# Kernel optimization log

Hardware: AMD Instinct MI355X
Metric: run time of the kernel (lower is better)

## Reference

```python
import jax, jax.numpy as jnp
import numpy as np

N, E, D, ED, H, OUT = 50000, 800000, 128, 32, 16, 128
BN_EPS = 1e-5


def setup_inputs() -> dict:
    key = jax.random.key(0)
    ks = jax.random.split(key, 12)
    s = lambda fan_in: 1.0 / np.sqrt(fan_in)

    x = jax.random.normal(ks[0], (N, D), dtype=jnp.float32)
    edge_idx = jax.random.randint(ks[1], (2, E), 0, N, dtype=jnp.int64)
    edge_feat = jax.random.normal(ks[2], (E, ED), dtype=jnp.float32)

    # edge_mlp: Linear(ED,16) -> GELU -> Linear(16,16); weights stored [in,out]
    eW1 = jax.random.uniform(ks[3], (ED, H), minval=-s(ED), maxval=s(ED), dtype=jnp.float32)
    eb1 = jnp.zeros((H,), jnp.float32)
    eW2 = jax.random.uniform(ks[4], (H, H), minval=-s(H), maxval=s(H), dtype=jnp.float32)
    eb2 = jnp.zeros((H,), jnp.float32)

    # ego_proj: Linear(D, D+16, bias=False)
    ego_W = jax.random.uniform(ks[5], (D, D + H), minval=-s(D), maxval=s(D), dtype=jnp.float32)
    eps = jnp.zeros((1,), jnp.float32)

    # node mlp: Linear(D+16, OUT) -> BN(OUT) -> GELU -> Linear(OUT, OUT)
    W1 = jax.random.uniform(ks[6], (D + H, OUT), minval=-s(D + H), maxval=s(D + H), dtype=jnp.float32)
    b1 = jnp.zeros((OUT,), jnp.float32)
    gamma = jnp.ones((OUT,), jnp.float32)
    beta = jnp.zeros((OUT,), jnp.float32)
    W2 = jax.random.uniform(ks[7], (OUT, OUT), minval=-s(OUT), maxval=s(OUT), dtype=jnp.float32)
    b2 = jnp.zeros((OUT,), jnp.float32)

    return dict(x=x, edge_idx=edge_idx, edge_feat=edge_feat,
                eW1=eW1, eb1=eb1, eW2=eW2, eb2=eb2,
                ego_W=ego_W, eps=eps,
                W1=W1, b1=b1, gamma=gamma, beta=beta, W2=W2, b2=b2)


def reference(x, edge_idx, edge_feat, eW1, eb1, eW2, eb2, ego_W, eps,
              W1, b1, gamma, beta, W2, b2):
    src, dst = edge_idx[0], edge_idx[1]
    # edge MLP (exact GELU, matching torch default)
    e_emb = jax.nn.gelu(edge_feat @ eW1 + eb1, approximate=False) @ eW2 + eb2  # [E,16]
    msg = jnp.concatenate([x[src], e_emb], axis=-1)                            # [E, D+16]
    agg = jax.ops.segment_sum(msg, dst, num_segments=x.shape[0])               # [N, D+16]
    out = (1.0 + eps) * (x @ ego_W) + agg
    # node MLP with BatchNorm1d in training mode (batch stats, biased var)
    h = out @ W1 + b1
    mu = jnp.mean(h, axis=0)
    var = jnp.mean((h - mu) ** 2, axis=0)
    h = (h - mu) * jax.lax.rsqrt(var + BN_EPS) * gamma + beta
    h = jax.nn.gelu(h, approximate=False)
    return h @ W2 + b2
```

## Files before the change

kernel.cpp:

```cpp
#include <hip/hip_runtime.h>
#include <hip/hip_bf16.h>

#define N_NODES 50000
#define E_EDGES 800000
#define D_IN    128
#define ED_IN   32
#define H_HID   16
#define D_CAT   144
#define AGG_LD  144
#define BCAP    48
#define BM      64
#define EDGE_BLKS (E_EDGES / 256)

typedef __attribute__((ext_vector_type(8))) short bf16x8;
typedef __attribute__((ext_vector_type(4))) float f32x4;

__device__ __forceinline__ float gelu_exact(float v) {
    return 0.5f * v * (1.0f + erff(v * 0.70710678118654752f));
}
__device__ __forceinline__ float4 ld4(const float* p) { return *reinterpret_cast<const float4*>(p); }
__device__ __forceinline__ unsigned short f2bf(float f) {
    unsigned u = __float_as_uint(f);
    return (unsigned short)((u + 0x7FFFu + ((u >> 16) & 1u)) >> 16);
}
__device__ __forceinline__ float bflo(unsigned u) { return __uint_as_float(u << 16); }
__device__ __forceinline__ float bfhi(unsigned u) { return __uint_as_float(u & 0xffff0000u); }
__device__ __forceinline__ unsigned packbf2(float lo, float hi) {
    __hip_bfloat162 h = __float22bfloat162_rn(make_float2(lo, hi));
    return *reinterpret_cast<unsigned*>(&h);
}

__global__ __launch_bounds__(256) void k_zero(int* __restrict__ cnt, float* __restrict__ stats) {
    int i = blockIdx.x * 256 + threadIdx.x;
    if (i < 12500) *reinterpret_cast<int4*>(cnt + i * 4) = make_int4(0, 0, 0, 0);
    if (blockIdx.x == 49 && threadIdx.x < 64)
        *reinterpret_cast<float4*>(stats + threadIdx.x * 4) = make_float4(0.f, 0.f, 0.f, 0.f);
}

__global__ __launch_bounds__(256) void k_edge(const float* __restrict__ x,
        uint4* __restrict__ xb, const int* __restrict__ eidx,
        const float* __restrict__ ef, const float* __restrict__ eW1,
        const float* __restrict__ eb1,
        const float* __restrict__ egoW, const float* __restrict__ W1,
        const float* __restrict__ eps, const float* __restrict__ eW2,
        const float* __restrict__ eb2, const float* __restrict__ W2,
        int* __restrict__ cnt, int* __restrict__ bucket,
        unsigned short* __restrict__ gbuf, unsigned short* __restrict__ BT,
        unsigned short* __restrict__ W2T, float* __restrict__ ve) {
    const int b = blockIdx.x, t = threadIdx.x;
    if (b >= EDGE_BLKS) {
        if (t >= 128) return;
        const int c = t;
        const int d = b - EDGE_BLKS;
        if (d < 128) {
            float acc = 0.f;
            for (int j = 0; j < D_CAT; ++j)
                acc = fmaf(egoW[d * D_CAT + j], W1[j * 128 + c], acc);
            BT[c * 288 + d] = f2bf((1.0f + eps[0]) * acc);
        } else if (d == 128) {
            for (int j = 0; j < 128; ++j)
                BT[c * 288 + 128 + j] = f2bf(W1[j * 128 + c]);
            #pragma unroll
            for (int j = 0; j < H_HID; ++j) {
                float s = 0.f;
                #pragma unroll
                for (int k = 0; k < H_HID; ++k)
                    s = fmaf(eW2[j * H_HID + k], W1[(D_IN + k) * 128 + c], s);
                BT[c * 288 + 256 + j] = f2bf(s);
            }
            #pragma unroll
            for (int j = 272; j < 288; ++j) BT[c * 288 + j] = 0;
            float s = 0.f;
            #pragma unroll
            for (int k = 0; k < H_HID; ++k)
                s = fmaf(eb2[k], W1[(D_IN + k) * 128 + c], s);
            ve[c] = s;
        } else {
            for (int k = 0; k < 128; ++k)
                W2T[c * 128 + k] = f2bf(W2[k * 128 + c]);
        }
        return;
    }
    const int e0 = b * 256;
    const int i = e0 + t;
    const int w = t >> 6, l = t & 63, q = l >> 4, c = l & 15;
    const int eb = e0 + w * 64;

    float4 cx0 = ld4(x + (size_t)i * 8);
    float4 cx1 = ld4(x + (size_t)i * 8 + 4);
    int dst = eidx[E_EDGES + i];
    float4 ef0[4], ef1[4];
    #pragma unroll
    for (int m = 0; m < 4; ++m) {
        const float* ep = ef + (size_t)(eb + m * 16 + c) * ED_IN + q * 8;
        ef0[m] = ld4(ep);
        ef1[m] = ld4(ep + 4);
    }
    float wv[8];
    #pragma unroll
    for (int j = 0; j < 8; ++j) wv[j] = eW1[(q * 8 + j) * 16 + c];
    union { uint4 u; bf16x8 v; } afc;
    afc.u.x = packbf2(wv[0], wv[1]); afc.u.y = packbf2(wv[2], wv[3]);
    afc.u.z = packbf2(wv[4], wv[5]); afc.u.w = packbf2(wv[6], wv[7]);
    const bf16x8 af = afc.v;
    float bias[4];
    #pragma unroll
    for (int j = 0; j < 4; ++j) bias[j] = eb1[q * 4 + j];

    {
        uint4 o;
        o.x = packbf2(cx0.x, cx0.y); o.y = packbf2(cx0.z, cx0.w);
        o.z = packbf2(cx1.x, cx1.y); o.w = packbf2(cx1.z, cx1.w);
        xb[i] = o;
    }
    {
        int pos = atomicAdd(&cnt[dst], 1);
        if (pos < BCAP) bucket[dst * BCAP + pos] = i;
    }
    #pragma unroll
    for (int m = 0; m < 4; ++m) {
        const int em = eb + m * 16 + c;
        union { uint4 u; bf16x8 v; } bc;
        bc.u.x = packbf2(ef0[m].x, ef0[m].y); bc.u.y = packbf2(ef0[m].z, ef0[m].w);
        bc.u.z = packbf2(ef1[m].x, ef1[m].y); bc.u.w = packbf2(ef1[m].z, ef1[m].w);
        f32x4 acc = (f32x4){0.f, 0.f, 0.f, 0.f};
        acc = __builtin_amdgcn_mfma_f32_16x16x32_bf16(af, bc.v, acc, 0, 0, 0);
        uint2 o;
        o.x = packbf2(gelu_exact(acc[0] + bias[0]), gelu_exact(acc[1] + bias[1]));
        o.y = packbf2(gelu_exact(acc[2] + bias[2]), gelu_exact(acc[3] + bias[3]));
        *reinterpret_cast<uint2*>(gbuf + (size_t)em * 16 + q * 4) = o;
    }
}

__global__ __launch_bounds__(256) void k_agg(const unsigned short* __restrict__ xb,
        const int* __restrict__ eidx, const int* __restrict__ cnt,
        const int* __restrict__ bucket, const unsigned short* __restrict__ gbuf,
        unsigned short* __restrict__ aggb) {
    const int wave = threadIdx.x >> 6, lane = threadIdx.x & 63;
    const int q = lane >> 4, ql = lane & 15;
    const int n = blockIdx.x * 4 + wave;
    const int m = min(cnt[n], BCAP);
    int ev = (lane < BCAP) ? bucket[n * BCAP + lane] : 0;
    int sv = (lane < m) ? eidx[ev] : 0;
    float a[8], ae[8];
    #pragma unroll
    for (int i = 0; i < 8; ++i) { a[i] = 0.f; ae[i] = 0.f; }
    const int ng = (m + 3) >> 2;
    #pragma unroll 4
    for (int j = 0; j < ng; ++j) {
        const int eo = 4 * j + q;
        const int s  = __shfl(sv, eo);
        const int ge = __shfl(ev, eo);
        if (eo < m) {
            uint4 v = *reinterpret_cast<const uint4*>(xb + (size_t)s * D_IN + ql * 8);
            a[0] += bflo(v.x); a[1] += bfhi(v.x);
            a[2] += bflo(v.y); a[3] += bfhi(v.y);
            a[4] += bflo(v.z); a[5] += bfhi(v.z);
            a[6] += bflo(v.w); a[7] += bfhi(v.w);
            if (ql < 2) {
                uint4 e = *reinterpret_cast<const uint4*>(gbuf + (size_t)ge * 16 + ql * 8);
                ae[0] += bflo(e.x); ae[1] += bfhi(e.x);
                ae[2] += bflo(e.y); ae[3] += bfhi(e.y);
                ae[4] += bflo(e.z); ae[5] += bfhi(e.z);
                ae[6] += bflo(e.w); ae[7] += bfhi(e.w);
            }
        }
    }
    #pragma unroll
    for (int i = 0; i < 8; ++i) {
        a[i]  += __shfl_xor(a[i], 16);  a[i]  += __shfl_xor(a[i], 32);
        ae[i] += __shfl_xor(ae[i], 16); ae[i] += __shfl_xor(ae[i], 32);
    }
    if (q == 0) {
        unsigned short* ar = aggb + (size_t)n * AGG_LD;
        uint4 o;
        o.x = packbf2(a[0], a[1]); o.y = packbf2(a[2], a[3]);
        o.z = packbf2(a[4], a[5]); o.w = packbf2(a[6], a[7]);
        *reinterpret_cast<uint4*>(ar + ql * 8) = o;
        if (ql < 2) {
            uint4 oe;
            oe.x = packbf2(ae[0], ae[1]); oe.y = packbf2(ae[2], ae[3]);
            oe.z = packbf2(ae[4], ae[5]); oe.w = packbf2(ae[6], ae[7]);
            *reinterpret_cast<uint4*>(ar + D_IN + ql * 8) = oe;
        }
    }
}

__global__ __launch_bounds__(256) void k_gemm1(const unsigned short* __restrict__ xb,
        const unsigned short* __restrict__ aggb, const unsigned short* __restrict__ BT,
        const float* __restrict__ ve, const int* __restrict__ cnt,
        float* __restrict__ h, float* __restrict__ stats) {
    __shared__ short As[64][40];
    __shared__ short Bs[128][40];
    __shared__ float red0[128], red1[128];
    __shared__ float ve_s[128];
    __shared__ int   deg_s[64];
    const int t = threadIdx.x;
    const int row0 = blockIdx.x * BM;
    if (t < 128) { ve_s[t] = ve[t]; red0[t] = 0.f; red1[t] = 0.f; }
    if (t < 64) deg_s[t] = cnt[min(row0 + t, N_NODES - 1)];
    const int w = t >> 6, l = t & 63;
    const int arow = w * 16 + (l & 15);
    const int koff = (l >> 4) * 8;
    f32x4 acc[8];
    #pragma unroll
    for (int ct = 0; ct < 8; ++ct) acc[ct] = (f32x4){0.f, 0.f, 0.f, 0.f};

    #pragma unroll 1
    for (int ch = 0; ch < 9; ++ch) {
        const unsigned short* Ab; int lda, k0, kb;
        if (ch < 4) { Ab = xb;   lda = D_IN;   k0 = ch * 32;       kb = ch * 32; }
        else        { Ab = aggb; lda = AGG_LD; k0 = (ch - 4) * 32; kb = 128 + (ch - 4) * 32; }
        {
            int row = t >> 2, slot = t & 3;
            int r = row0 + row;
            uint4 v = make_uint4(0u, 0u, 0u, 0u);
            if (r < N_NODES) v = *reinterpret_cast<const uint4*>(Ab + (size_t)r * lda + k0 + slot * 8);
            *reinterpret_cast<uint4*>(&As[row][slot * 8]) = v;
        }
        #pragma unroll
        for (int i = 0; i < 2; ++i) {
            int qq = t + 256 * i;
            int row = qq >> 2, slot = qq & 3;
            *reinterpret_cast<uint4*>(&Bs[row][slot * 8]) =
                *reinterpret_cast<const uint4*>(BT + row * 288 + kb + slot * 8);
        }
        __syncthreads();
        bf16x8 af = *reinterpret_cast<const bf16x8*>(&As[arow][koff]);
        #pragma unroll
        for (int ct = 0; ct < 8; ++ct) {
            bf16x8 bfv = *reinterpret_cast<const bf16x8*>(&Bs[ct * 16 + (l & 15)][koff]);
            acc[ct] = __builtin_amdgcn_mfma_f32_16x16x32_bf16(af, bfv, acc[ct], 0, 0, 0);
        }
        __syncthreads();
    }

    #pragma unroll
    for (int ct = 0; ct < 8; ++ct) {
        const int col = ct * 16 + (l & 15);
        float cs0 = 0.f, cs1 = 0.f;
        #pragma unroll
        for (int i = 0; i < 4; ++i) {
            int lr = w * 16 + (l >> 4) * 4 + i;
            int r = row0 + lr;
            float dv = (float)deg_s[lr];
            float v = acc[ct][i] + dv * ve_s[col];
            if (r < N_NODES) { h[(size_t)r * 128 + col] = v; cs0 += v; cs1 += v * v; }
        }
        cs0 += __shfl_xor(cs0, 16); cs0 += __shfl_xor(cs0, 32);
        cs1 += __shfl_xor(cs1, 16); cs1 += __shfl_xor(cs1, 32);
        if (l < 16) { atomicAdd(&red0[col], cs0); atomicAdd(&red1[col], cs1); }
    }
    __syncthreads();
    if (t < 128) {
        unsafeAtomicAdd(stats + t,       red0[t]);
        unsafeAtomicAdd(stats + 128 + t, red1[t]);
    }
}

__global__ __launch_bounds__(256) void k_gemm2(const float* __restrict__ h,
        const float* __restrict__ stats, const float* __restrict__ gamma,
        const float* __restrict__ beta, const unsigned short* __restrict__ W2T,
        const float* __restrict__ b2, float* __restrict__ out) {
    __shared__ short As[64][136];
    __shared__ short Bs[128][40];
    __shared__ float sa[128], sb[128], sc[128];
    const int t = threadIdx.x;
    const int row0 = blockIdx.x * BM;
    if (t < 128) {
        float mu  = stats[t] * (1.0f / N_NODES);
        float var = stats[128 + t] * (1.0f / N_NODES) - mu * mu;
        float av  = gamma[t] * rsqrtf(var + 1e-5f);
        sa[t] = av;
        sb[t] = beta[t] - mu * av;
        sc[t] = b2[t];
    }
    __syncthreads();
    {
        int row = t >> 2, q = t & 3;
        int r = row0 + row;
        #pragma unroll
        for (int i = 0; i < 8; ++i) {
            int c = q * 32 + i * 4;
            float4 v = (r < N_NODES) ? ld4(h + (size_t)r * 128 + c) : make_float4(0.f, 0.f, 0.f, 0.f);
            uint2 pw;
            pw.x = packbf2(gelu_exact(fmaf(sa[c],     v.x, sb[c])),
                           gelu_exact(fmaf(sa[c + 1], v.y, sb[c + 1])));
            pw.y = packbf2(gelu_exact(fmaf(sa[c + 2], v.z, sb[c + 2])),
                           gelu_exact(fmaf(sa[c + 3], v.w, sb[c + 3])));
            *reinterpret_cast<uint2*>(&As[row][c]) = pw;
        }
    }
    const int w = t >> 6, l = t & 63;
    const int arow = w * 16 + (l & 15);
    const int koff = (l >> 4) * 8;
    f32x4 acc[8];
    #pragma unroll
    for (int ct = 0; ct < 8; ++ct) acc[ct] = (f32x4){0.f, 0.f, 0.f, 0.f};

    #pragma unroll 1
    for (int ks = 0; ks < 4; ++ks) {
        #pragma unroll
        for (int i = 0; i < 2; ++i) {
            int qq = t + 256 * i;
            int row = qq >> 2, slot = qq & 3;
            *reinterpret_cast<uint4*>(&Bs[row][slot * 8]) =
                *reinterpret_cast<const uint4*>(W2T + row * 128 + ks * 32 + slot * 8);
        }
        __syncthreads();
        bf16x8 af = *reinterpret_cast<const bf16x8*>(&As[arow][ks * 32 + koff]);
        #pragma unroll
        for (int ct = 0; ct < 8; ++ct) {
            bf16x8 bfv = *reinterpret_cast<const bf16x8*>(&Bs[ct * 16 + (l & 15)][koff]);
            acc[ct] = __builtin_amdgcn_mfma_f32_16x16x32_bf16(af, bfv, acc[ct], 0, 0, 0);
        }
        __syncthreads();
    }
    #pragma unroll
    for (int ct = 0; ct < 8; ++ct) {
        const int col = ct * 16 + (l & 15);
        #pragma unroll
        for (int i = 0; i < 4; ++i) {
            int r = row0 + w * 16 + (l >> 4) * 4 + i;
            if (r < N_NODES) out[(size_t)r * 128 + col] = acc[ct][i] + sc[col];
        }
    }
}

extern "C" void kernel_launch(void* const* d_in, const int* in_sizes, int n_in,
                              void* d_out, int out_size, void* d_ws, size_t ws_size,
                              hipStream_t stream) {
    const float* x     = (const float*)d_in[0];
    const int*   eidx  = (const int*)d_in[1];
    const float* ef    = (const float*)d_in[2];
    const float* eW1   = (const float*)d_in[3];
    const float* eb1   = (const float*)d_in[4];
    const float* eW2   = (const float*)d_in[5];
    const float* eb2   = (const float*)d_in[6];
    const float* egoW  = (const float*)d_in[7];
    const float* eps   = (const float*)d_in[8];
    const float* W1    = (const float*)d_in[9];
    const float* gamma = (const float*)d_in[11];
    const float* beta  = (const float*)d_in[12];
    const float* W2    = (const float*)d_in[13];
    const float* b2    = (const float*)d_in[14];
    float* out = (float*)d_out;

    char* ws = (char*)d_ws;
    unsigned short* aggb = (unsigned short*)ws;
    unsigned short* xb   = (unsigned short*)(ws + 14400128);
    float* stats  = (float*)(ws + 27200128);
    unsigned short* BT  = (unsigned short*)(ws + 27201152);
    unsigned short* W2T = (unsigned short*)(ws + 27274880);
    float* ve     = (float*)(ws + 27307648);
    int*   cnt    = (int*)(ws + 27308160);
    int*   bucket = (int*)(ws + 27508864);
    unsigned short* gbuf = (unsigned short*)d_out;
    float* h      = out;

    k_zero<<<dim3(50), dim3(256), 0, stream>>>(cnt, stats);
    k_edge<<<dim3(EDGE_BLKS + 130), dim3(256), 0, stream>>>(x, (uint4*)xb, eidx, ef, eW1, eb1,
                                                            egoW, W1, eps, eW2, eb2, W2,
                                                            cnt, bucket, gbuf, BT, W2T, ve);
    k_agg<<<dim3(N_NODES / 4), dim3(256), 0, stream>>>(xb, eidx, cnt, bucket, gbuf, aggb);
    k_gemm1<<<dim3((N_NODES + BM - 1) / BM), dim3(256), 0, stream>>>(xb, aggb, BT, ve,
                                                                     cnt, h, stats);
    k_gemm2<<<dim3((N_NODES + BM - 1) / BM), dim3(256), 0, stream>>>(h, stats, gamma, beta,
                                                                     W2T, b2, out);
}
```

Baseline: 170.0 us.

## Fuse neighbor aggregation into GEMM1 and store pre-BN activations in bf16

Merges the gather-aggregate kernel into the first GEMM. Each block now aggregates neighbor features for its 64 rows directly into a full-width shared A tile holding x, the aggregate and the edge embedding, so the aggregate no longer makes a round trip through global memory. The intermediate h is also stored as bf16 instead of fp32, which halves the traffic between GEMM1 and GEMM2. The trade-off is that only 782 blocks each serially process 16 rows per wave during aggregation, which lowers memory-level parallelism for the latency-bound gather. The large shared tile (about 40KB) may also reduce occupancy, and h loses precision before BatchNorm.

```diff
diff --git a/kernel.cpp b/kernel.cpp
--- a/kernel.cpp
+++ b/kernel.cpp
@@ -7,10 +7,10 @@
 #define ED_IN   32
 #define H_HID   16
 #define D_CAT   144
-#define AGG_LD  144
 #define BCAP    48
 #define BM      64
 #define EDGE_BLKS (E_EDGES / 256)
+#define ALD     312
 
 typedef __attribute__((ext_vector_type(8))) short bf16x8;
 typedef __attribute__((ext_vector_type(4))) float f32x4;
@@ -132,65 +132,12 @@
     }
 }
 
-__global__ __launch_bounds__(256) void k_agg(const unsigned short* __restrict__ xb,
+__global__ __launch_bounds__(256) void k_fuse(const unsigned short* __restrict__ xb,
         const int* __restrict__ eidx, const int* __restrict__ cnt,
         const int* __restrict__ bucket, const unsigned short* __restrict__ gbuf,
-        unsigned short* __restrict__ aggb) {
-    const int wave = threadIdx.x >> 6, lane = threadIdx.x & 63;
-    const int q = lane >> 4, ql = lane & 15;
-    const int n = blockIdx.x * 4 + wave;
-    const int m = min(cnt[n], BCAP);
-    int ev = (lane < BCAP) ? bucket[n * BCAP + lane] : 0;
-    int sv = (lane < m) ? eidx[ev] : 0;
-    float a[8], ae[8];
-    #pragma unroll
-    for (int i = 0; i < 8; ++i) { a[i] = 0.f; ae[i] = 0.f; }
-    const int ng = (m + 3) >> 2;
-    #pragma unroll 4
-    for (int j = 0; j < ng; ++j) {
-        const int eo = 4 * j + q;
-        const int s  = __shfl(sv, eo);
-        const int ge = __shfl(ev, eo);
-        if (eo < m) {
-            uint4 v = *reinterpret_cast<const uint4*>(xb + (size_t)s * D_IN + ql * 8);
-            a[0] += bflo(v.x); a[1] += bfhi(v.x);
-            a[2] += bflo(v.y); a[3] += bfhi(v.y);
-            a[4] += bflo(v.z); a[5] += bfhi(v.z);
-            a[6] += bflo(v.w); a[7] += bfhi(v.w);
-            if (ql < 2) {
-                uint4 e = *reinterpret_cast<const uint4*>(gbuf + (size_t)ge * 16 + ql * 8);
-                ae[0] += bflo(e.x); ae[1] += bfhi(e.x);
-                ae[2] += bflo(e.y); ae[3] += bfhi(e.y);
-                ae[4] += bflo(e.z); ae[5] += bfhi(e.z);
-                ae[6] += bflo(e.w); ae[7] += bfhi(e.w);
-            }
-        }
-    }
-    #pragma unroll
-    for (int i = 0; i < 8; ++i) {
-        a[i]  += __shfl_xor(a[i], 16);  a[i]  += __shfl_xor(a[i], 32);
-        ae[i] += __shfl_xor(ae[i], 16); ae[i] += __shfl_xor(ae[i], 32);
-    }
-    if (q == 0) {
-        unsigned short* ar = aggb + (size_t)n * AGG_LD;
-        uint4 o;
-        o.x = packbf2(a[0], a[1]); o.y = packbf2(a[2], a[3]);
-        o.z = packbf2(a[4], a[5]); o.w = packbf2(a[6], a[7]);
-        *reinterpret_cast<uint4*>(ar + ql * 8) = o;
-        if (ql < 2) {
-            uint4 oe;
-            oe.x = packbf2(ae[0], ae[1]); oe.y = packbf2(ae[2], ae[3]);
-            oe.z = packbf2(ae[4], ae[5]); oe.w = packbf2(ae[6], ae[7]);
-            *reinterpret_cast<uint4*>(ar + D_IN + ql * 8) = oe;
-        }
-    }
-}
-
-__global__ __launch_bounds__(256) void k_gemm1(const unsigned short* __restrict__ xb,
-        const unsigned short* __restrict__ aggb, const unsigned short* __restrict__ BT,
-        const float* __restrict__ ve, const int* __restrict__ cnt,
-        float* __restrict__ h, float* __restrict__ stats) {
-    __shared__ short As[64][40];
+        const unsigned short* __restrict__ BT, const float* __restrict__ ve,
+        unsigned short* __restrict__ h, float* __restrict__ stats) {
+    __shared__ short As[64][ALD];
     __shared__ short Bs[128][40];
     __shared__ float red0[128], red1[128];
     __shared__ float ve_s[128];
@@ -198,38 +145,98 @@
     const int t = threadIdx.x;
     const int row0 = blockIdx.x * BM;
     if (t < 128) { ve_s[t] = ve[t]; red0[t] = 0.f; red1[t] = 0.f; }
-    if (t < 64) deg_s[t] = cnt[min(row0 + t, N_NODES - 1)];
-    const int w = t >> 6, l = t & 63;
-    const int arow = w * 16 + (l & 15);
-    const int koff = (l >> 4) * 8;
+    if (t < 64) deg_s[t] = (row0 + t < N_NODES) ? cnt[row0 + t] : 0;
+    {
+        const int row = t >> 2, slot = t & 3;
+        const int r = row0 + row;
+        #pragma unroll
+        for (int j = 0; j < 4; ++j) {
+            uint4 v = make_uint4(0u, 0u, 0u, 0u);
+            if (r < N_NODES)
+                v = *reinterpret_cast<const uint4*>(xb + (size_t)r * 128 + slot * 32 + j * 8);
+            *reinterpret_cast<uint4*>(&As[row][slot * 32 + j * 8]) = v;
+        }
+    }
+    __syncthreads();
+
+    const int w = t >> 6, l = t & 63, q = l >> 4, ql = l & 15;
+    for (int k = 0; k < 16; ++k) {
+        const int lr = w * 16 + k;
+        const int n = row0 + lr;
+        const int m = (n < N_NODES) ? min(deg_s[lr], BCAP) : 0;
+        if (m == 0) {
+            if (q == 0) {
+                uint4 z = make_uint4(0u, 0u, 0u, 0u);
+                *reinterpret_cast<uint4*>(&As[lr][128 + ql * 8]) = z;
+                if (ql < 4) *reinterpret_cast<uint4*>(&As[lr][256 + ql * 8]) = z;
+            }
+            continue;
+        }
+        int ev = (l < BCAP) ? bucket[n * BCAP + l] : 0;
+        int sv = (l < m) ? eidx[ev] : 0;
+        float a[8], ae[8];
+        #pragma unroll
+        for (int i = 0; i < 8; ++i) { a[i] = 0.f; ae[i] = 0.f; }
+        const int ng = (m + 3) >> 2;
+        for (int j = 0; j < ng; ++j) {
+            const int eo = 4 * j + q;
+            const int s  = __shfl(sv, eo);
+            const int ge = __shfl(ev, eo);
+            if (eo < m) {
+                uint4 v = *reinterpret_cast<const uint4*>(xb + (size_t)s * D_IN + ql * 8);
+                a[0] += bflo(v.x); a[1] += bfhi(v.x);
+                a[2] += bflo(v.y); a[3] += bfhi(v.y);
+                a[4] += bflo(v.z); a[5] += bfhi(v.z);
+                a[6] += bflo(v.w); a[7] += bfhi(v.w);
+                if (ql < 2) {
+                    uint4 e = *reinterpret_cast<const uint4*>(gbuf + (size_t)ge * 16 + ql * 8);
+                    ae[0] += bflo(e.x); ae[1] += bfhi(e.x);
+                    ae[2] += bflo(e.y); ae[3] += bfhi(e.y);
+                    ae[4] += bflo(e.z); ae[5] += bfhi(e.z);
+                    ae[6] += bflo(e.w); ae[7] += bfhi(e.w);
+                }
+            }
+        }
+        #pragma unroll
+        for (int i = 0; i < 8; ++i) {
+            a[i]  += __shfl_xor(a[i], 16);  a[i]  += __shfl_xor(a[i], 32);
+            ae[i] += __shfl_xor(ae[i], 16); ae[i] += __shfl_xor(ae[i], 32);
+        }
+        if (q == 0) {
+            uint4 o;
+            o.x = packbf2(a[0], a[1]); o.y = packbf2(a[2], a[3]);
+            o.z = packbf2(a[4], a[5]); o.w = packbf2(a[6], a[7]);
+            *reinterpret_cast<uint4*>(&As[lr][128 + ql * 8]) = o;
+            if (ql < 2) {
+                uint4 oe;
+                oe.x = packbf2(ae[0], ae[1]); oe.y = packbf2(ae[2], ae[3]);
+                oe.z = packbf2(ae[4], ae[5]); oe.w = packbf2(ae[6], ae[7]);
+                *reinterpret_cast<uint4*>(&As[lr][256 + ql * 8]) = oe;
+            } else if (ql < 4) {
+                uint4 z = make_uint4(0u, 0u, 0u, 0u);
+                *reinterpret_cast<uint4*>(&As[lr][256 + ql * 8]) = z;
+            }
+        }
+    }
+    __syncthreads();
+
     f32x4 acc[8];
     #pragma unroll
     for (int ct = 0; ct < 8; ++ct) acc[ct] = (f32x4){0.f, 0.f, 0.f, 0.f};
-
     #pragma unroll 1
     for (int ch = 0; ch < 9; ++ch) {
-        const unsigned short* Ab; int lda, k0, kb;
-        if (ch < 4) { Ab = xb;   lda = D_IN;   k0 = ch * 32;       kb = ch * 32; }
-        else        { Ab = aggb; lda = AGG_LD; k0 = (ch - 4) * 32; kb = 128 + (ch - 4) * 32; }
-        {
-            int row = t >> 2, slot = t & 3;
-            int r = row0 + row;
-            uint4 v = make_uint4(0u, 0u, 0u, 0u);
-            if (r < N_NODES) v = *reinterpret_cast<const uint4*>(Ab + (size_t)r * lda + k0 + slot * 8);
-            *reinterpret_cast<uint4*>(&As[row][slot * 8]) = v;
-        }
         #pragma unroll
         for (int i = 0; i < 2; ++i) {
             int qq = t + 256 * i;
-            int row = qq >> 2, slot = qq & 3;
-            *reinterpret_cast<uint4*>(&Bs[row][slot * 8]) =
-                *reinterpret_cast<const uint4*>(BT + row * 288 + kb + slot * 8);
+            int brow = qq >> 2, bslot = qq & 3;
+            *reinterpret_cast<uint4*>(&Bs[brow][bslot * 8]) =
+                *reinterpret_cast<const uint4*>(BT + brow * 288 + ch * 32 + bslot * 8);
         }
         __syncthreads();
-        bf16x8 af = *reinterpret_cast<const bf16x8*>(&As[arow][koff]);
+        bf16x8 af = *reinterpret_cast<const bf16x8*>(&As[w * 16 + ql][ch * 32 + q * 8]);
         #pragma unroll
         for (int ct = 0; ct < 8; ++ct) {
-            bf16x8 bfv = *reinterpret_cast<const bf16x8*>(&Bs[ct * 16 + (l & 15)][koff]);
+            bf16x8 bfv = *reinterpret_cast<const bf16x8*>(&Bs[ct * 16 + ql][q * 8]);
             acc[ct] = __builtin_amdgcn_mfma_f32_16x16x32_bf16(af, bfv, acc[ct], 0, 0, 0);
         }
         __syncthreads();
@@ -237,15 +244,15 @@
 
     #pragma unroll
     for (int ct = 0; ct < 8; ++ct) {
-        const int col = ct * 16 + (l & 15);
+        const int col = ct * 16 + ql;
         float cs0 = 0.f, cs1 = 0.f;
         #pragma unroll
         for (int i = 0; i < 4; ++i) {
-            int lr = w * 16 + (l >> 4) * 4 + i;
+            int lr = w * 16 + q * 4 + i;
             int r = row0 + lr;
             float dv = (float)deg_s[lr];
             float v = acc[ct][i] + dv * ve_s[col];
-            if (r < N_NODES) { h[(size_t)r * 128 + col] = v; cs0 += v; cs1 += v * v; }
+            if (r < N_NODES) { h[(size_t)r * 128 + col] = f2bf(v); cs0 += v; cs1 += v * v; }
         }
         cs0 += __shfl_xor(cs0, 16); cs0 += __shfl_xor(cs0, 32);
         cs1 += __shfl_xor(cs1, 16); cs1 += __shfl_xor(cs1, 32);
@@ -258,7 +265,7 @@
     }
 }
 
-__global__ __launch_bounds__(256) void k_gemm2(const float* __restrict__ h,
+__global__ __launch_bounds__(256) void k_gemm2(const unsigned short* __restrict__ h,
         const float* __restrict__ stats, const float* __restrict__ gamma,
         const float* __restrict__ beta, const unsigned short* __restrict__ W2T,
         const float* __restrict__ b2, float* __restrict__ out) {
@@ -277,18 +284,25 @@
     }
     __syncthreads();
     {
-        int row = t >> 2, q = t & 3;
-        int r = row0 + row;
-        #pragma unroll
-        for (int i = 0; i < 8; ++i) {
-            int c = q * 32 + i * 4;
-            float4 v = (r < N_NODES) ? ld4(h + (size_t)r * 128 + c) : make_float4(0.f, 0.f, 0.f, 0.f);
-            uint2 pw;
-            pw.x = packbf2(gelu_exact(fmaf(sa[c],     v.x, sb[c])),
-                           gelu_exact(fmaf(sa[c + 1], v.y, sb[c + 1])));
-            pw.y = packbf2(gelu_exact(fmaf(sa[c + 2], v.z, sb[c + 2])),
-                           gelu_exact(fmaf(sa[c + 3], v.w, sb[c + 3])));
-            *reinterpret_cast<uint2*>(&As[row][c]) = pw;
+        const int row = t >> 2, q2 = t & 3;
+        const int r = row0 + row;
+        #pragma unroll
+        for (int i = 0; i < 4; ++i) {
+            const int c = q2 * 32 + i * 8;
+            uint4 v = make_uint4(0u, 0u, 0u, 0u);
+            if (r < N_NODES) v = *reinterpret_cast<const uint4*>(h + (size_t)r * 128 + c);
+            float f0 = bflo(v.x), f1 = bfhi(v.x), f2 = bflo(v.y), f3 = bfhi(v.y);
+            float f4 = bflo(v.z), f5 = bfhi(v.z), f6 = bflo(v.w), f7 = bfhi(v.w);
+            uint4 o;
+            o.x = packbf2(gelu_exact(fmaf(sa[c],     f0, sb[c])),
+                          gelu_exact(fmaf(sa[c + 1], f1, sb[c + 1])));
+            o.y = packbf2(gelu_exact(fmaf(sa[c + 2], f2, sb[c + 2])),
+                          gelu_exact(fmaf(sa[c + 3], f3, sb[c + 3])));
+            o.z = packbf2(gelu_exact(fmaf(sa[c + 4], f4, sb[c + 4])),
+                          gelu_exact(fmaf(sa[c + 5], f5, sb[c + 5])));
+            o.w = packbf2(gelu_exact(fmaf(sa[c + 6], f6, sb[c + 6])),
+                          gelu_exact(fmaf(sa[c + 7], f7, sb[c + 7])));
+            *reinterpret_cast<uint4*>(&As[row][c]) = o;
         }
     }
     const int w = t >> 6, l = t & 63;
@@ -347,24 +361,22 @@
     float* out = (float*)d_out;
 
     char* ws = (char*)d_ws;
-    unsigned short* aggb = (unsigned short*)ws;
-    unsigned short* xb   = (unsigned short*)(ws + 14400128);
-    float* stats  = (float*)(ws + 27200128);
-    unsigned short* BT  = (unsigned short*)(ws + 27201152);
-    unsigned short* W2T = (unsigned short*)(ws + 27274880);
-    float* ve     = (float*)(ws + 27307648);
-    int*   cnt    = (int*)(ws + 27308160);
-    int*   bucket = (int*)(ws + 27508864);
+    unsigned short* xb  = (unsigned short*)ws;
+    unsigned short* h   = (unsigned short*)(ws + 12800000);
+    float* stats  = (float*)(ws + 25600000);
+    unsigned short* BT  = (unsigned short*)(ws + 25601024);
+    unsigned short* W2T = (unsigned short*)(ws + 25674752);
+    float* ve     = (float*)(ws + 25707520);
+    int*   cnt    = (int*)(ws + 25708032);
+    int*   bucket = (int*)(ws + 25908224);
     unsigned short* gbuf = (unsigned short*)d_out;
-    float* h      = out;
 
     k_zero<<<dim3(50), dim3(256), 0, stream>>>(cnt, stats);
     k_edge<<<dim3(EDGE_BLKS + 130), dim3(256), 0, stream>>>(x, (uint4*)xb, eidx, ef, eW1, eb1,
                                                             egoW, W1, eps, eW2, eb2, W2,
                                                             cnt, bucket, gbuf, BT, W2T, ve);
-    k_agg<<<dim3(N_NODES / 4), dim3(256), 0, stream>>>(xb, eidx, cnt, bucket, gbuf, aggb);
-    k_gemm1<<<dim3((N_NODES + BM - 1) / BM), dim3(256), 0, stream>>>(xb, aggb, BT, ve,
-                                                                     cnt, h, stats);
+    k_fuse<<<dim3((N_NODES + BM - 1) / BM), dim3(256), 0, stream>>>(xb, eidx, cnt, bucket,
+                                                                    gbuf, BT, ve, h, stats);
     k_gemm2<<<dim3((N_NODES + BM - 1) / BM), dim3(256), 0, stream>>>(h, stats, gamma, beta,
                                                                      W2T, b2, out);
 }
```

New measurement: 215.4 us. 26.7% more time.
